# Kernel optimization log

Hardware: AMD Instinct MI355X
Metric: run time of the kernel (lower is better)

## Reference

```python
import jax, jax.numpy as jnp
import numpy as np

DEPTH = 3


def _gather_nei(feats, graph):
    # feats: [B, M, F], graph: [B, N, NB] -> [B, N, NB, F]
    return jax.vmap(lambda f, g: f[g])(feats, graph)


def setup_inputs() -> dict:
    B, N, NB, NBOND = 64, 120, 10, 250
    AF, BF, H = 82, 6, 300
    key = jax.random.key(0)
    ks = jax.random.split(key, 14)
    inp = {
        "atom_feats_1": jax.random.normal(ks[0], (B, N, AF), dtype=jnp.float32),
        "bond_feats": jax.random.normal(ks[1], (B, NBOND, BF), dtype=jnp.float32),
        "atom_graph": jax.random.randint(ks[2], (B, N, NB), 0, N, dtype=jnp.int64),
        "bond_graph": jax.random.randint(ks[3], (B, N, NB), 0, NBOND, dtype=jnp.int64),
        "num_nbs": jax.random.randint(ks[4], (B, N), 0, NB, dtype=jnp.int64),
        "n_atoms": jax.random.randint(ks[5], (B,), 1, N, dtype=jnp.int64),
        "mask_neis": jax.random.randint(ks[6], (B, N, NB, 1), 0, 2) > 0,
        "mask_atoms": jax.random.randint(ks[7], (B, N, 1), 0, 2) > 0,
        # parameters (Linear weights stored as [in, out]); dropout is eval-mode (identity)
        "W_fc1": jax.random.normal(ks[8], (AF, H), dtype=jnp.float32) * 0.05,
        "W_gc_nei": jax.random.normal(ks[9], (H + BF, H), dtype=jnp.float32) * 0.05,
        "b_gc_nei": jnp.zeros((H,), dtype=jnp.float32),
        "W_gc_atom": jax.random.normal(ks[10], (2 * H, H), dtype=jnp.float32) * 0.05,
        "b_gc_atom": jnp.zeros((H,), dtype=jnp.float32),
        "W_fc2a": jax.random.normal(ks[11], (H, H), dtype=jnp.float32) * 0.05,
        "W_fc2b": jax.random.normal(ks[12], (BF, H), dtype=jnp.float32) * 0.05,
        "W_fc2": jax.random.normal(ks[13], (H, H), dtype=jnp.float32) * 0.05,
    }
    return inp


def reference(atom_feats_1, bond_feats, atom_graph, bond_graph, num_nbs, n_atoms,
              mask_neis, mask_atoms, W_fc1, W_gc_nei, b_gc_nei, W_gc_atom,
              b_gc_atom, W_fc2a, W_fc2b, W_fc2):
    zero = jnp.float32(0)
    atom_feats = jax.nn.relu(atom_feats_1 @ W_fc1)                 # [B,N,H]
    bondnei_feats = _gather_nei(bond_feats, bond_graph)            # [B,N,NB,BF]
    local_feats = None
    for i in range(DEPTH):
        atomnei_feats = _gather_nei(atom_feats, atom_graph)        # [B,N,NB,H]
        if i + 1 == DEPTH:
            an = atomnei_feats @ W_fc2a                            # [B,N,NB,H]
            bn = bondnei_feats @ W_fc2b                            # [B,N,NB,H]
            nei = jnp.where(mask_neis, an * bn, zero).sum(-2)      # [B,N,H]
            self_feats = atom_feats @ W_fc2                        # [B,N,H]
            local_feats = jnp.where(mask_atoms, self_feats * nei, zero)
        else:
            cat = jnp.concatenate([atomnei_feats, bondnei_feats], axis=-1)
            nei = jax.nn.relu(cat @ W_gc_nei + b_gc_nei)           # [B,N,NB,H]
            nei = jnp.where(mask_neis, nei, zero).sum(-2)          # [B,N,H]
            update = jnp.concatenate([atom_feats, nei], axis=-1)   # [B,N,2H]
            atom_feats = jax.nn.relu(update @ W_gc_atom + b_gc_atom)
    return local_feats
```

## Files before the change

### kernel.cpp

```cpp
#include <hip/hip_runtime.h>
#include <hip/hip_bf16.h>

#define BATCH 64
#define NATOM 120
#define NNB 10
#define NBOND 250
#define AFDIM 82
#define BFDIM 6
#define HREAL 300
#define HP 320
#define NCT32 10
#define MA (BATCH*NATOM)
#define MB (BATCH*NBOND)

typedef short short8 __attribute__((ext_vector_type(8)));
typedef float f32x16 __attribute__((ext_vector_type(16)));
typedef unsigned int u32;
typedef u32 u32x2 __attribute__((ext_vector_type(2)));
typedef unsigned short u16;
typedef unsigned char u8;

__device__ __forceinline__ float bflo(u32 v) { return __builtin_bit_cast(float, v << 16); }
__device__ __forceinline__ float bfhi(u32 v) { return __builtin_bit_cast(float, v & 0xffff0000u); }
__device__ __forceinline__ float bfu(u16 v) { return __builtin_bit_cast(float, (u32)v << 16); }
__device__ __forceinline__ u16 f2bf(float f) {
    __hip_bfloat16 h = __float2bfloat16(f);
    return __builtin_bit_cast(u16, h);
}
__device__ __forceinline__ int imin(int a, int b) { return a < b ? a : b; }

struct PackJob { const float* W; short8* dst; int Kreal, KT, KTfull, ktOff, blk0; };
struct Prep {
    const int *mn, *agp, *bgp; u32* pk;
    PackJob j[6];
};

#define PACK_BLKS 265
#define PK_BASE   PACK_BLKS
#define PK_BLKS   300
#define PREP_BLKS (PK_BASE + PK_BLKS)

__global__ __launch_bounds__(256) void prep_all(Prep cfg) {
    const int bid = blockIdx.x;
    const int tid = threadIdx.x;
    if (bid < PK_BASE) {
        int ji = 0;
#pragma unroll
        for (int i = 1; i < 6; ++i) if (bid >= cfg.j[i].blk0) ji = i;
        const PackJob J = cfg.j[ji];
        int id = (bid - J.blk0) * 256 + tid;
        int n = NCT32 * J.KT * 64;
        if (id >= n) return;
        int lane = id & 63;
        int kt = (id >> 6) % J.KT;
        int ct = id / (J.KT * 64);
        int col = ct * 32 + (lane & 31);
        int kbase = kt * 16 + (lane >> 5) * 8;
        short8 v;
#pragma unroll
        for (int jj = 0; jj < 8; ++jj) {
            int k = kbase + jj;
            float f = (k < J.Kreal && col < HREAL) ? J.W[(size_t)k * HREAL + col] : 0.f;
            v[jj] = (short)f2bf(f);
        }
        J.dst[(size_t)(ct * J.KTfull + J.ktOff + kt) * 64 + lane] = v;
    } else {
        int id = (bid - PK_BASE) * 256 + tid;
        u32 w = 0;
        if (cfg.mn[id]) w = 0x80000000u | ((u32)cfg.agp[id] << 16) | (u32)cfg.bgp[id];
        cfg.pk[id] = w;
    }
}

__global__ __launch_bounds__(128)
void k_fc1(const float* __restrict__ A1,
           const short8* __restrict__ pW1,
           __hip_bfloat16* __restrict__ af0) {
    __shared__ short8 Wl[2 * 6 * 64];
    const int tid  = threadIdx.x;
    const int lane = tid & 63;
    const int wv   = tid >> 6;
    const int m0   = blockIdx.x * 64 + wv * 32;
    const int ct0  = blockIdx.y * 2;
    const int r1   = m0 + (lane & 31);
    const int koff = (lane >> 5) * 8;

    {
        const short8* wsrc = pW1 + (size_t)ct0 * 6 * 64;
#pragma unroll
        for (int i = 0; i < 6; ++i) Wl[i * 128 + tid] = wsrc[i * 128 + tid];
    }
    __syncthreads();

    const float* src = A1 + (size_t)r1 * AFDIM;
    short8 a[6];
#pragma unroll
    for (int g = 0; g < 6; ++g) {
#pragma unroll
        for (int j = 0; j < 8; ++j) {
            const int k = g * 16 + koff + j;
            const float f = (k < AFDIM) ? src[k] : 0.f;
            a[g][j] = (short)f2bf(f);
        }
    }

    f32x16 acc[2];
#pragma unroll
    for (int r = 0; r < 16; ++r) { acc[0][r] = 0.f; acc[1][r] = 0.f; }
    const short8* w0 = Wl + lane;
    const short8* w1 = Wl + 6 * 64 + lane;
#pragma unroll
    for (int g = 0; g < 6; ++g) {
        acc[0] = __builtin_amdgcn_mfma_f32_32x32x16_bf16(a[g], w0[g * 64], acc[0], 0, 0, 0);
        acc[1] = __builtin_amdgcn_mfma_f32_32x32x16_bf16(a[g], w1[g * 64], acc[1], 0, 0, 0);
    }
#pragma unroll
    for (int c = 0; c < 2; ++c) {
        const int col = (ct0 + c) * 32 + (lane & 31);
#pragma unroll
        for (int r = 0; r < 16; ++r) {
            const int row = m0 + (r & 3) + 8 * (r >> 2) + 4 * (lane >> 5);
            af0[(size_t)row * HP + col] = __float2bfloat16(fmaxf(acc[c][r], 0.f));
        }
    }
}

#define BOT_LDS (2 * 40 * 64 * 16)
__global__ __launch_bounds__(256)
void k_gemm_bot(const __hip_bfloat16* __restrict__ af,
                const __hip_bfloat16* __restrict__ neib,
                const short8* __restrict__ W,
                const float* __restrict__ b_ga,
                __hip_bfloat16* __restrict__ afn) {
    extern __shared__ short8 Wl[];
    const int tid  = threadIdx.x;
    const int lane = tid & 63;
    const int wv   = tid >> 6;
    const int m0   = blockIdx.x * 128 + wv * 32;
    const int ct0  = blockIdx.y * 2;
    const int r1   = m0 + (lane & 31);
    const int koff = (lane >> 5) * 8;

    {
        const short8* wsrc = W + (size_t)ct0 * 40 * 64;
#pragma unroll
        for (int i = 0; i < 20; ++i) Wl[i * 256 + tid] = wsrc[i * 256 + tid];
    }
    __syncthreads();

    f32x16 acc[2];
#pragma unroll
    for (int r = 0; r < 16; ++r) { acc[0][r] = 0.f; acc[1][r] = 0.f; }
    const short8* w0 = Wl + lane;
    const short8* w1 = Wl + 40 * 64 + lane;

#pragma unroll
    for (int ch = 0; ch < 4; ++ch) {
        short8 a[10];
#pragma unroll
        for (int kt = 0; kt < 10; ++kt) {
            const int g = ch * 10 + kt;
            if (g < 20)
                a[kt] = *reinterpret_cast<const short8*>(af + (size_t)r1 * HP + g * 16 + koff);
            else
                a[kt] = *reinterpret_cast<const short8*>(neib + (size_t)r1 * HP + (g - 20) * 16 + koff);
        }
#pragma unroll
        for (int kt = 0; kt < 10; ++kt) {
            const int g = ch * 10 + kt;
            acc[0] = __builtin_amdgcn_mfma_f32_32x32x16_bf16(a[kt], w0[g * 64], acc[0], 0, 0, 0);
            acc[1] = __builtin_amdgcn_mfma_f32_32x32x16_bf16(a[kt], w1[g * 64], acc[1], 0, 0, 0);
        }
    }

#pragma unroll
    for (int c = 0; c < 2; ++c) {
        const int col = (ct0 + c) * 32 + (lane & 31);
        const float bb = (col < HREAL) ? b_ga[col] : 0.f;
#pragma unroll
        for (int r = 0; r < 16; ++r) {
            const int row = m0 + (r & 3) + 8 * (r >> 2) + 4 * (lane >> 5);
            afn[(size_t)row * HP + col] = __float2bfloat16(fmaxf(acc[c][r] + bb, 0.f));
        }
    }
}

#define NUG_LDS (20480 + 7680 + 16000 + 4800 + 4000 + 384)
__global__ __launch_bounds__(256)
void k_nu_gather(const __hip_bfloat16* __restrict__ af,
                 const short8* __restrict__ pWnei,
                 const float* __restrict__ bond,
                 const float* __restrict__ Wgn_bond,
                 const float* __restrict__ b_gn,
                 const u32* __restrict__ pk,
                 u32* __restrict__ nei) {
    extern __shared__ char smraw[];
    short8* WL  = (short8*)smraw;
    u16*    TL  = (u16*)(smraw + 20480);
    u16*    BLh = (u16*)(smraw + 28160);
    u32*    PL  = (u32*)(smraw + 44160);
    u16*    BFL = (u16*)(smraw + 48960);
    u16*    WS  = (u16*)(smraw + 52960);
    u32*    BL  = (u32*)BLh;
    const int b   = blockIdx.x;
    const int ct  = blockIdx.y;
    const int tid = threadIdx.x;

    {
        const short8* wsrc = pWnei + (size_t)ct * 20 * 64;
#pragma unroll
        for (int i = 0; i < 5; ++i) WL[i * 256 + tid] = wsrc[i * 256 + tid];
    }
    for (int i = tid; i < NBOND * 8; i += 256) {
        const int r = i >> 3, k = i & 7;
        const float f = (k < BFDIM) ? bond[(size_t)(b * NBOND + r) * BFDIM + k] : 0.f;
        BFL[i] = f2bf(f);
    }
    if (tid < 192) {
        const int k = tid >> 5, c = tid & 31;
        const int col = ct * 32 + c;
        const float f = (col < HREAL) ? Wgn_bond[(size_t)k * HREAL + col] : 0.f;
        WS[tid] = f2bf(f);
    }
    for (int i = tid; i < NATOM * NNB; i += 256) PL[i] = pk[b * NATOM * NNB + i];
    __syncthreads();

    for (int i = tid; i < NBOND * 16; i += 256) {
        const int r = i >> 4, cp = i & 15;
        const int col0 = ct * 32 + 2 * cp;
        float lo = 0.f, hi = 0.f;
#pragma unroll
        for (int k = 0; k < BFDIM; ++k) {
            const float bv = bfu(BFL[r * 8 + k]);
            const u32 wv2 = *reinterpret_cast<const u32*>(&WS[k * 32 + 2 * cp]);
            lo += bv * bflo(wv2);
            hi += bv * bfhi(wv2);
        }
        const float v0 = (col0     < HREAL) ? lo + b_gn[col0]     : 0.f;
        const float v1 = (col0 + 1 < HREAL) ? hi + b_gn[col0 + 1] : 0.f;
        BL[r * 16 + cp] = (u32)f2bf(v0) | ((u32)f2bf(v1) << 16);
    }

    {
        const int lane = tid & 63;
        const int wv   = tid >> 6;
        const int r1   = imin(wv * 32 + (lane & 31), NATOM - 1);
        const int koff = (lane >> 5) * 8;
        const __hip_bfloat16* arow = af + (size_t)(b * NATOM + r1) * HP + koff;
        f32x16 acc;
#pragma unroll
        for (int r = 0; r < 16; ++r) acc[r] = 0.f;
        const short8* w0 = WL + lane;
#pragma unroll
        for (int ch = 0; ch < 2; ++ch) {
            short8 a[10];
#pragma unroll
            for (int kt = 0; kt < 10; ++kt)
                a[kt] = *reinterpret_cast<const short8*>(arow + (ch * 10 + kt) * 16);
#pragma unroll
            for (int kt = 0; kt < 10; ++kt)
                acc = __builtin_amdgcn_mfma_f32_32x32x16_bf16(a[kt], w0[(ch * 10 + kt) * 64], acc, 0, 0, 0);
        }
        const int col = lane & 31;
#pragma unroll
        for (int r = 0; r < 16; ++r) {
            const int row = wv * 32 + (r & 3) + 8 * (r >> 2) + 4 * (lane >> 5);
            if (row < NATOM) TL[row * 32 + col] = f2bf(acc[r]);
        }
    }
    __syncthreads();

    for (int i = tid; i < NATOM * 16; i += 256) {
        const int row = i >> 4, cp = i & 15;
        float lo = 0.f, hi = 0.f;
#pragma unroll
        for (int j = 0; j < NNB; ++j) {
            const u32 w = PL[row * NNB + j];
            if ((int)w < 0) {
                const int a  = (w >> 16) & 0xff;
                const int bo = w & 0xffff;
                const u32 ta = *reinterpret_cast<const u32*>(&TL[a * 32 + 2 * cp]);
                const u32 tb = BL[bo * 16 + cp];
                lo += fmaxf(bflo(ta) + bflo(tb), 0.f);
                hi += fmaxf(bfhi(ta) + bfhi(tb), 0.f);
            }
        }
        nei[(size_t)(b * NATOM + row) * (HP / 2) + ct * 16 + cp] =
            (u32)f2bf(lo) | ((u32)f2bf(hi) << 16);
    }
}

#define FIN_LDS (40960 + 7680 + 7680 + 16000 + 4800 + 120 + 4000 + 384)
__global__ __launch_bounds__(256)
void k_final_fused(const __hip_bfloat16* __restrict__ af,
                   const short8* __restrict__ pWfd,
                   const float* __restrict__ bond,
                   const float* __restrict__ W_fc2b,
                   const u32* __restrict__ pk,
                   const int* __restrict__ maska,
                   float* __restrict__ out) {
    extern __shared__ char smraw[];
    short8* WL  = (short8*)smraw;
    u16*    SL  = (u16*)(smraw + 40960);
    u16*    AL  = (u16*)(smraw + 48640);
    u16*    BLh = (u16*)(smraw + 56320);
    u32*    PL  = (u32*)(smraw + 72320);
    u8*     ML  = (u8*)(smraw + 77120);
    u16*    BFL = (u16*)(smraw + 77240);
    u16*    WS  = (u16*)(smraw + 81240);
    u32*    BL  = (u32*)BLh;
    const int b   = blockIdx.x;
    const int ct  = blockIdx.y;
    const int tid = threadIdx.x;

    {
        const short8* w2  = pWfd + (size_t)ct * 20 * 64;
        const short8* w2a = pWfd + (size_t)(NCT32 + ct) * 20 * 64;
#pragma unroll
        for (int i = 0; i < 5; ++i) {
            WL[i * 256 + tid]        = w2[i * 256 + tid];
            WL[1280 + i * 256 + tid] = w2a[i * 256 + tid];
        }
    }
    for (int i = tid; i < NBOND * 8; i += 256) {
        const int r = i >> 3, k = i & 7;
        const float f = (k < BFDIM) ? bond[(size_t)(b * NBOND + r) * BFDIM + k] : 0.f;
        BFL[i] = f2bf(f);
    }
    if (tid < 192) {
        const int k = tid >> 5, c = tid & 31;
        const int col = ct * 32 + c;
        const float f = (col < HREAL) ? W_fc2b[(size_t)k * HREAL + col] : 0.f;
        WS[tid] = f2bf(f);
    }
    for (int i = tid; i < NATOM * NNB; i += 256) PL[i] = pk[b * NATOM * NNB + i];
    for (int i = tid; i < NATOM; i += 256) ML[i] = (u8)(maska[b * NATOM + i] != 0);
    __syncthreads();

    for (int i = tid; i < NBOND * 16; i += 256) {
        const int r = i >> 4, cp = i & 15;
        float lo = 0.f, hi = 0.f;
#pragma unroll
        for (int k = 0; k < BFDIM; ++k) {
            const float bv = bfu(BFL[r * 8 + k]);
            const u32 wv2 = *reinterpret_cast<const u32*>(&WS[k * 32 + 2 * cp]);
            lo += bv * bflo(wv2);
            hi += bv * bfhi(wv2);
        }
        BL[r * 16 + cp] = (u32)f2bf(lo) | ((u32)f2bf(hi) << 16);
    }

    {
        const int lane = tid & 63;
        const int wv   = tid >> 6;
        const int r1   = imin(wv * 32 + (lane & 31), NATOM - 1);
        const int koff = (lane >> 5) * 8;
        const __hip_bfloat16* arow = af + (size_t)(b * NATOM + r1) * HP + koff;
        f32x16 acc0, acc1;
#pragma unroll
        for (int r = 0; r < 16; ++r) { acc0[r] = 0.f; acc1[r] = 0.f; }
        const short8* w0 = WL + lane;
        const short8* w1 = WL + 1280 + lane;
#pragma unroll
        for (int ch = 0; ch < 2; ++ch) {
            short8 a[10];
#pragma unroll
            for (int kt = 0; kt < 10; ++kt)
                a[kt] = *reinterpret_cast<const short8*>(arow + (ch * 10 + kt) * 16);
#pragma unroll
            for (int kt = 0; kt < 10; ++kt) {
                acc0 = __builtin_amdgcn_mfma_f32_32x32x16_bf16(a[kt], w0[(ch * 10 + kt) * 64], acc0, 0, 0, 0);
                acc1 = __builtin_amdgcn_mfma_f32_32x32x16_bf16(a[kt], w1[(ch * 10 + kt) * 64], acc1, 0, 0, 0);
            }
        }
        const int col = lane & 31;
#pragma unroll
        for (int r = 0; r < 16; ++r) {
            const int row = wv * 32 + (r & 3) + 8 * (r >> 2) + 4 * (lane >> 5);
            if (row < NATOM) {
                SL[row * 32 + col] = f2bf(acc0[r]);
                AL[row * 32 + col] = f2bf(acc1[r]);
            }
        }
    }
    __syncthreads();

    for (int i = tid; i < NATOM * 16; i += 256) {
        const int row = i >> 4, cp = i & 15;
        const int c = ct * 32 + 2 * cp;
        if (c >= HREAL) continue;
        float lo = 0.f, hi = 0.f;
#pragma unroll
        for (int j = 0; j < NNB; ++j) {
            const u32 w = PL[row * NNB + j];
            if ((int)w < 0) {
                const int a  = (w >> 16) & 0xff;
                const int bo = w & 0xffff;
                const u32 va = *reinterpret_cast<const u32*>(&AL[a * 32 + 2 * cp]);
                const u32 vb = BL[bo * 16 + cp];
                lo += bflo(va) * bflo(vb);
                hi += bfhi(va) * bfhi(vb);
            }
        }
        float2 r2;
        r2.x = 0.f; r2.y = 0.f;
        if (ML[row]) {
            const u32 s = *reinterpret_cast<const u32*>(&SL[row * 32 + 2 * cp]);
            r2.x = bflo(s) * lo;
            r2.y = bfhi(s) * hi;
        }
        *reinterpret_cast<float2*>(out + (size_t)(b * NATOM + row) * HREAL + c) = r2;
    }
}

extern "C" void kernel_launch(void* const* d_in, const int* in_sizes, int n_in,
                              void* d_out, int out_size, void* d_ws, size_t ws_size,
                              hipStream_t stream) {
    const float* A1        = (const float*)d_in[0];
    const float* bond      = (const float*)d_in[1];
    const int*   ag        = (const int*)d_in[2];
    const int*   bg        = (const int*)d_in[3];
    const int*   maskn     = (const int*)d_in[6];
    const int*   maska     = (const int*)d_in[7];
    const float* W_fc1     = (const float*)d_in[8];
    const float* W_gc_nei  = (const float*)d_in[9];
    const float* b_gc_nei  = (const float*)d_in[10];
    const float* W_gc_atom = (const float*)d_in[11];
    const float* b_gc_atom = (const float*)d_in[12];
    const float* W_fc2a    = (const float*)d_in[13];
    const float* W_fc2b    = (const float*)d_in[14];
    const float* W_fc2     = (const float*)d_in[15];
    float* out = (float*)d_out;

    char* p = (char*)d_ws;
    auto alloc = [&](size_t bytes) { char* r = p; p += (bytes + 63) & ~(size_t)63; return r; };
    __hip_bfloat16* af0    = (__hip_bfloat16*)alloc((size_t)MA * HP * 2);
    __hip_bfloat16* af1    = (__hip_bfloat16*)alloc((size_t)MA * HP * 2);
    __hip_bfloat16* neib   = (__hip_bfloat16*)alloc((size_t)MA * HP * 2);
    u32*            pk     = (u32*)alloc((size_t)MA * NNB * 4);
    short8* pW1  = (short8*)alloc((size_t)NCT32 * 6  * 64 * 16);
    short8* pWnei= (short8*)alloc((size_t)NCT32 * 20 * 64 * 16);
    short8* pWga = (short8*)alloc((size_t)NCT32 * 40 * 64 * 16);
    short8* pWfd = (short8*)alloc((size_t)2 * NCT32 * 20 * 64 * 16);

    Prep cfg;
    cfg.mn = maskn; cfg.agp = ag; cfg.bgp = bg; cfg.pk = pk;
    cfg.j[0] = { W_fc1,                             pW1,                         AFDIM, 6,  6,  0,   0 };
    cfg.j[1] = { W_gc_nei,                          pWnei,                       HREAL, 20, 20, 0,  15 };
    cfg.j[2] = { W_gc_atom,                         pWga,                        HREAL, 20, 40, 0,  65 };
    cfg.j[3] = { W_gc_atom + (size_t)HREAL * HREAL, pWga,                        HREAL, 20, 40, 20, 115 };
    cfg.j[4] = { W_fc2,                             pWfd,                        HREAL, 20, 20, 0, 165 };
    cfg.j[5] = { W_fc2a,                            pWfd + (size_t)NCT32*20*64,  HREAL, 20, 20, 0, 215 };
    prep_all<<<dim3(PREP_BLKS), dim3(256), 0, stream>>>(cfg);

    static int attr_done = 0;
    if (!attr_done) {
        hipFuncSetAttribute((const void*)k_gemm_bot,    hipFuncAttributeMaxDynamicSharedMemorySize, BOT_LDS);
        hipFuncSetAttribute((const void*)k_final_fused, hipFuncAttributeMaxDynamicSharedMemorySize, FIN_LDS);
        attr_done = 1;
    }

    k_fc1<<<dim3(MA / 64, 5), dim3(128), 0, stream>>>(A1, pW1, af0);

    const dim3 gNUG(BATCH, NCT32);
    const dim3 gBOT(MA / 128, 5);
    const dim3 t256(256);
    const float* Wgn_bond = W_gc_nei + (size_t)HREAL * HREAL;

    const __hip_bfloat16* af = af0;
    __hip_bfloat16* afn = af1;
    for (int it = 0; it < 2; ++it) {
        k_nu_gather<<<gNUG, t256, NUG_LDS, stream>>>(
            af, pWnei, bond, Wgn_bond, b_gc_nei, pk, (u32*)neib);
        k_gemm_bot<<<gBOT, t256, BOT_LDS, stream>>>(af, neib, pWga, b_gc_atom, afn);
        const __hip_bfloat16* t = afn; afn = (__hip_bfloat16*)af; af = t;
    }

    k_final_fused<<<gNUG, t256, FIN_LDS, stream>>>(
        af, pWfd, bond, W_fc2b, pk, maska, out);
}
```

Before: 141.6 us.

## Pack neighbor indices to 16 bits and cut final kernel LDS footprint

```diff
diff --git a/kernel.cpp b/kernel.cpp
--- a/kernel.cpp
+++ b/kernel.cpp
@@ -31,7 +31,7 @@
 
 struct PackJob { const float* W; short8* dst; int Kreal, KT, KTfull, ktOff, blk0; };
 struct Prep {
-    const int *mn, *agp, *bgp; u32* pk;
+    const int *mn, *agp, *bgp; u16* pk16;
     PackJob j[6];
 };
 
@@ -66,9 +66,10 @@
         J.dst[(size_t)(ct * J.KTfull + J.ktOff + kt) * 64 + lane] = v;
     } else {
         int id = (bid - PK_BASE) * 256 + tid;
-        u32 w = 0;
-        if (cfg.mn[id]) w = 0x80000000u | ((u32)cfg.agp[id] << 16) | (u32)cfg.bgp[id];
-        cfg.pk[id] = w;
+        u16 w = 0;
+        if (cfg.mn[id])
+            w = (u16)(0x8000u | ((u32)cfg.agp[id] << 8) | (u32)cfg.bgp[id]);
+        cfg.pk16[id] = w;
     }
 }
 
@@ -185,23 +186,22 @@
     }
 }
 
-#define NUG_LDS (20480 + 7680 + 16000 + 4800 + 4000 + 384)
+#define NUG_LDS (20480 + 7680 + 16000 + 2400 + 4000 + 384)
 __global__ __launch_bounds__(256)
 void k_nu_gather(const __hip_bfloat16* __restrict__ af,
                  const short8* __restrict__ pWnei,
                  const float* __restrict__ bond,
                  const float* __restrict__ Wgn_bond,
                  const float* __restrict__ b_gn,
-                 const u32* __restrict__ pk,
+                 const u16* __restrict__ pk16,
                  u32* __restrict__ nei) {
     extern __shared__ char smraw[];
     short8* WL  = (short8*)smraw;
     u16*    TL  = (u16*)(smraw + 20480);
-    u16*    BLh = (u16*)(smraw + 28160);
-    u32*    PL  = (u32*)(smraw + 44160);
-    u16*    BFL = (u16*)(smraw + 48960);
-    u16*    WS  = (u16*)(smraw + 52960);
-    u32*    BL  = (u32*)BLh;
+    u32*    BL  = (u32*)(smraw + 28160);
+    u16*    PLh = (u16*)(smraw + 44160);
+    u16*    BFL = (u16*)(smraw + 46560);
+    u16*    WS  = (u16*)(smraw + 50560);
     const int b   = blockIdx.x;
     const int ct  = blockIdx.y;
     const int tid = threadIdx.x;
@@ -222,7 +222,8 @@
         const float f = (col < HREAL) ? Wgn_bond[(size_t)k * HREAL + col] : 0.f;
         WS[tid] = f2bf(f);
     }
-    for (int i = tid; i < NATOM * NNB; i += 256) PL[i] = pk[b * NATOM * NNB + i];
+    for (int i = tid; i < 600; i += 256)
+        reinterpret_cast<u32*>(PLh)[i] = reinterpret_cast<const u32*>(pk16)[(size_t)b * 600 + i];
     __syncthreads();
 
     for (int i = tid; i < NBOND * 16; i += 256) {
@@ -275,10 +276,10 @@
         float lo = 0.f, hi = 0.f;
 #pragma unroll
         for (int j = 0; j < NNB; ++j) {
-            const u32 w = PL[row * NNB + j];
-            if ((int)w < 0) {
-                const int a  = (w >> 16) & 0xff;
-                const int bo = w & 0xffff;
+            const u16 w = PLh[row * NNB + j];
+            if (w & 0x8000) {
+                const int a  = (w >> 8) & 0x7f;
+                const int bo = w & 0xff;
                 const u32 ta = *reinterpret_cast<const u32*>(&TL[a * 32 + 2 * cp]);
                 const u32 tb = BL[bo * 16 + cp];
                 lo += fmaxf(bflo(ta) + bflo(tb), 0.f);
@@ -290,37 +291,34 @@
     }
 }
 
-#define FIN_LDS (40960 + 7680 + 7680 + 16000 + 4800 + 120 + 4000 + 384)
+#define FIN_LDS (20480 + 7680 + 16000 + 2400 + 120 + 4000 + 384)
 __global__ __launch_bounds__(256)
 void k_final_fused(const __hip_bfloat16* __restrict__ af,
                    const short8* __restrict__ pWfd,
                    const float* __restrict__ bond,
                    const float* __restrict__ W_fc2b,
-                   const u32* __restrict__ pk,
+                   const u16* __restrict__ pk16,
                    const int* __restrict__ maska,
                    float* __restrict__ out) {
     extern __shared__ char smraw[];
     short8* WL  = (short8*)smraw;
-    u16*    SL  = (u16*)(smraw + 40960);
-    u16*    AL  = (u16*)(smraw + 48640);
-    u16*    BLh = (u16*)(smraw + 56320);
-    u32*    PL  = (u32*)(smraw + 72320);
-    u8*     ML  = (u8*)(smraw + 77120);
-    u16*    BFL = (u16*)(smraw + 77240);
-    u16*    WS  = (u16*)(smraw + 81240);
-    u32*    BL  = (u32*)BLh;
+    u16*    AL  = (u16*)(smraw + 20480);
+    u32*    BL  = (u32*)(smraw + 28160);
+    u16*    PLh = (u16*)(smraw + 44160);
+    u8*     ML  = (u8*)(smraw + 46560);
+    u16*    BFL = (u16*)(smraw + 46680);
+    u16*    WS  = (u16*)(smraw + 50680);
+    float*  GL  = (float*)smraw;
     const int b   = blockIdx.x;
     const int ct  = blockIdx.y;
     const int tid = threadIdx.x;
-
-    {
-        const short8* w2  = pWfd + (size_t)ct * 20 * 64;
+    const int lane = tid & 63;
+    const int wv   = tid >> 6;
+
+    {
         const short8* w2a = pWfd + (size_t)(NCT32 + ct) * 20 * 64;
 #pragma unroll
-        for (int i = 0; i < 5; ++i) {
-            WL[i * 256 + tid]        = w2[i * 256 + tid];
-            WL[1280 + i * 256 + tid] = w2a[i * 256 + tid];
-        }
+        for (int i = 0; i < 5; ++i) WL[i * 256 + tid] = w2a[i * 256 + tid];
     }
     for (int i = tid; i < NBOND * 8; i += 256) {
         const int r = i >> 3, k = i & 7;
@@ -333,7 +331,8 @@
         const float f = (col < HREAL) ? W_fc2b[(size_t)k * HREAL + col] : 0.f;
         WS[tid] = f2bf(f);
     }
-    for (int i = tid; i < NATOM * NNB; i += 256) PL[i] = pk[b * NATOM * NNB + i];
+    for (int i = tid; i < 600; i += 256)
+        reinterpret_cast<u32*>(PLh)[i] = reinterpret_cast<const u32*>(pk16)[(size_t)b * 600 + i];
     for (int i = tid; i < NATOM; i += 256) ML[i] = (u8)(maska[b * NATOM + i] != 0);
     __syncthreads();
 
@@ -350,17 +349,14 @@
         BL[r * 16 + cp] = (u32)f2bf(lo) | ((u32)f2bf(hi) << 16);
     }
 
-    {
-        const int lane = tid & 63;
-        const int wv   = tid >> 6;
-        const int r1   = imin(wv * 32 + (lane & 31), NATOM - 1);
-        const int koff = (lane >> 5) * 8;
-        const __hip_bfloat16* arow = af + (size_t)(b * NATOM + r1) * HP + koff;
-        f32x16 acc0, acc1;
-#pragma unroll
-        for (int r = 0; r < 16; ++r) { acc0[r] = 0.f; acc1[r] = 0.f; }
+    const int r1   = imin(wv * 32 + (lane & 31), NATOM - 1);
+    const int koff = (lane >> 5) * 8;
+    const __hip_bfloat16* arow = af + (size_t)(b * NATOM + r1) * HP + koff;
+    {
+        f32x16 acc1;
+#pragma unroll
+        for (int r = 0; r < 16; ++r) acc1[r] = 0.f;
         const short8* w0 = WL + lane;
-        const short8* w1 = WL + 1280 + lane;
 #pragma unroll
         for (int ch = 0; ch < 2; ++ch) {
             short8 a[10];
@@ -368,48 +364,76 @@
             for (int kt = 0; kt < 10; ++kt)
                 a[kt] = *reinterpret_cast<const short8*>(arow + (ch * 10 + kt) * 16);
 #pragma unroll
-            for (int kt = 0; kt < 10; ++kt) {
-                acc0 = __builtin_amdgcn_mfma_f32_32x32x16_bf16(a[kt], w0[(ch * 10 + kt) * 64], acc0, 0, 0, 0);
-                acc1 = __builtin_amdgcn_mfma_f32_32x32x16_bf16(a[kt], w1[(ch * 10 + kt) * 64], acc1, 0, 0, 0);
-            }
+            for (int kt = 0; kt < 10; ++kt)
+                acc1 = __builtin_amdgcn_mfma_f32_32x32x16_bf16(a[kt], w0[(ch * 10 + kt) * 64], acc1, 0, 0, 0);
         }
         const int col = lane & 31;
 #pragma unroll
         for (int r = 0; r < 16; ++r) {
             const int row = wv * 32 + (r & 3) + 8 * (r >> 2) + 4 * (lane >> 5);
-            if (row < NATOM) {
-                SL[row * 32 + col] = f2bf(acc0[r]);
-                AL[row * 32 + col] = f2bf(acc1[r]);
-            }
+            if (row < NATOM) AL[row * 32 + col] = f2bf(acc1[r]);
+        }
+    }
+    __syncthreads();
+
+    {
+        const short8* w2 = pWfd + (size_t)ct * 20 * 64;
+#pragma unroll
+        for (int i = 0; i < 5; ++i) WL[i * 256 + tid] = w2[i * 256 + tid];
+    }
+    __syncthreads();
+
+    f32x16 acc0;
+#pragma unroll
+    for (int r = 0; r < 16; ++r) acc0[r] = 0.f;
+    {
+        const short8* w0 = WL + lane;
+#pragma unroll
+        for (int ch = 0; ch < 2; ++ch) {
+            short8 a[10];
+#pragma unroll
+            for (int kt = 0; kt < 10; ++kt)
+                a[kt] = *reinterpret_cast<const short8*>(arow + (ch * 10 + kt) * 16);
+#pragma unroll
+            for (int kt = 0; kt < 10; ++kt)
+                acc0 = __builtin_amdgcn_mfma_f32_32x32x16_bf16(a[kt], w0[(ch * 10 + kt) * 64], acc0, 0, 0, 0);
         }
     }
     __syncthreads();
 
     for (int i = tid; i < NATOM * 16; i += 256) {
         const int row = i >> 4, cp = i & 15;
-        const int c = ct * 32 + 2 * cp;
-        if (c >= HREAL) continue;
         float lo = 0.f, hi = 0.f;
 #pragma unroll
         for (int j = 0; j < NNB; ++j) {
-            const u32 w = PL[row * NNB + j];
-            if ((int)w < 0) {
-                const int a  = (w >> 16) & 0xff;
-                const int bo = w & 0xffff;
+            const u16 w = PLh[row * NNB + j];
+            if (w & 0x8000) {
+                const int a  = (w >> 8) & 0x7f;
+                const int bo = w & 0xff;
                 const u32 va = *reinterpret_cast<const u32*>(&AL[a * 32 + 2 * cp]);
                 const u32 vb = BL[bo * 16 + cp];
                 lo += bflo(va) * bflo(vb);
                 hi += bfhi(va) * bfhi(vb);
             }
         }
-        float2 r2;
-        r2.x = 0.f; r2.y = 0.f;
-        if (ML[row]) {
-            const u32 s = *reinterpret_cast<const u32*>(&SL[row * 32 + 2 * cp]);
-            r2.x = bflo(s) * lo;
-            r2.y = bfhi(s) * hi;
-        }
-        *reinterpret_cast<float2*>(out + (size_t)(b * NATOM + row) * HREAL + c) = r2;
+        GL[row * 32 + 2 * cp]     = lo;
+        GL[row * 32 + 2 * cp + 1] = hi;
+    }
+    __syncthreads();
+
+    {
+        const int col = ct * 32 + (lane & 31);
+        if (col < HREAL) {
+#pragma unroll
+            for (int r = 0; r < 16; ++r) {
+                const int row = wv * 32 + (r & 3) + 8 * (r >> 2) + 4 * (lane >> 5);
+                if (row < NATOM) {
+                    float v = 0.f;
+                    if (ML[row]) v = bfu(f2bf(acc0[r])) * GL[row * 32 + (lane & 31)];
+                    out[(size_t)(b * NATOM + row) * HREAL + col] = v;
+                }
+            }
+        }
     }
 }
 
@@ -437,14 +461,14 @@
     __hip_bfloat16* af0    = (__hip_bfloat16*)alloc((size_t)MA * HP * 2);
     __hip_bfloat16* af1    = (__hip_bfloat16*)alloc((size_t)MA * HP * 2);
     __hip_bfloat16* neib   = (__hip_bfloat16*)alloc((size_t)MA * HP * 2);
-    u32*            pk     = (u32*)alloc((size_t)MA * NNB * 4);
+    u16*            pk16   = (u16*)alloc((size_t)MA * NNB * 2);
     short8* pW1  = (short8*)alloc((size_t)NCT32 * 6  * 64 * 16);
     short8* pWnei= (short8*)alloc((size_t)NCT32 * 20 * 64 * 16);
     short8* pWga = (short8*)alloc((size_t)NCT32 * 40 * 64 * 16);
     short8* pWfd = (short8*)alloc((size_t)2 * NCT32 * 20 * 64 * 16);
 
     Prep cfg;
-    cfg.mn = maskn; cfg.agp = ag; cfg.bgp = bg; cfg.pk = pk;
+    cfg.mn = maskn; cfg.agp = ag; cfg.bgp = bg; cfg.pk16 = pk16;
     cfg.j[0] = { W_fc1,                             pW1,                         AFDIM, 6,  6,  0,   0 };
     cfg.j[1] = { W_gc_nei,                          pWnei,                       HREAL, 20, 20, 0,  15 };
     cfg.j[2] = { W_gc_atom,                         pWga,                        HREAL, 20, 40, 0,  65 };
@@ -455,8 +479,7 @@
 
     static int attr_done = 0;
     if (!attr_done) {
-        hipFuncSetAttribute((const void*)k_gemm_bot,    hipFuncAttributeMaxDynamicSharedMemorySize, BOT_LDS);
-        hipFuncSetAttribute((const void*)k_final_fused, hipFuncAttributeMaxDynamicSharedMemorySize, FIN_LDS);
+        hipFuncSetAttribute((const void*)k_gemm_bot, hipFuncAttributeMaxDynamicSharedMemorySize, BOT_LDS);
         attr_done = 1;
     }
 
@@ -471,11 +494,11 @@
     __hip_bfloat16* afn = af1;
     for (int it = 0; it < 2; ++it) {
         k_nu_gather<<<gNUG, t256, NUG_LDS, stream>>>(
-            af, pWnei, bond, Wgn_bond, b_gc_nei, pk, (u32*)neib);
+            af, pWnei, bond, Wgn_bond, b_gc_nei, pk16, (u32*)neib);
         k_gemm_bot<<<gBOT, t256, BOT_LDS, stream>>>(af, neib, pWga, b_gc_atom, afn);
         const __hip_bfloat16* t = afn; afn = (__hip_bfloat16*)af; af = t;
     }
 
     k_final_fused<<<gNUG, t256, FIN_LDS, stream>>>(
-        af, pWfd, bond, W_fc2b, pk, maska, out);
-}
+        af, pWfd, bond, W_fc2b, pk16, maska, out);
+}
```

Measured after the change: 129.4 us. 8.7% less time.
